# Kernel optimization log

Measured on AMD Instinct MI355X. Metric: run time of the kernel, lower is better.

The kernel has to match this reference:

```python
import jax, jax.numpy as jnp
import numpy as np

N = 8192        # nodes
E = 49152       # edges (~avg degree 6, triangular mesh)
H = 6           # GATv2 heads
C = 512         # hidden_size (per-head out channels)
F_IN = 2 + C    # GATv2 in_channels = coord(2) + hidden(512)
ALL_FEAT = 37   # deform_in_c-2 + 16 + 16
NUM_LOOP = 3
LRELU_SLOPE = 0.2


def setup_inputs() -> dict:
    key = jax.random.key(0)
    ks = jax.random.split(key, 10)
    x = jax.random.uniform(ks[0], (N, 7), dtype=jnp.float32)
    local_feat = jax.random.normal(ks[1], (N, 16), dtype=jnp.float32)
    conv_feat = jax.random.normal(ks[2], (N, 16), dtype=jnp.float32)
    edge_index = jax.random.randint(ks[3], (2, E), 0, N, dtype=jnp.int64)
    bd_mask = jnp.zeros((N,), jnp.int32)  # poly_mesh=False path
    W_lin = jax.random.normal(ks[4], (ALL_FEAT, C), dtype=jnp.float32) / np.float32(np.sqrt(ALL_FEAT))
    b_lin = jnp.zeros((C,), jnp.float32)
    Wl = jax.random.normal(ks[5], (F_IN, H * C), dtype=jnp.float32) / np.float32(np.sqrt(F_IN))
    Wr = jax.random.normal(ks[6], (F_IN, H * C), dtype=jnp.float32) / np.float32(np.sqrt(F_IN))
    att = jax.random.normal(ks[7], (H, C), dtype=jnp.float32) / np.float32(np.sqrt(C))
    gat_bias = jnp.zeros((C,), jnp.float32)
    W_coord = jax.random.normal(ks[8], (C, 2), dtype=jnp.float32) / np.float32(np.sqrt(C))
    b_coord = jnp.zeros((2,), jnp.float32)
    return dict(x=x, local_feat=local_feat, conv_feat=conv_feat,
                W_lin=W_lin, b_lin=b_lin, Wl=Wl, Wr=Wr, att=att,
                gat_bias=gat_bias, W_coord=W_coord, b_coord=b_coord,
                edge_index=edge_index, bd_mask=bd_mask)


def _gatv2(feat, src, dst, Wl, Wr, att, bias):
    # PyG GATv2Conv: lin_l on source, lin_r on target, additive attention
    n = feat.shape[0]
    xl = (feat @ Wl).reshape(n, H, C)            # source-side transform
    xr = (feat @ Wr).reshape(n, H, C)            # target-side transform
    e = xl[src] + xr[dst]                        # [E', H, C]
    e = jax.nn.leaky_relu(e, LRELU_SLOPE)
    logits = jnp.einsum('ehc,hc->eh', e, att)    # [E', H]
    m = jax.ops.segment_max(logits, dst, num_segments=n)
    m = jnp.where(jnp.isfinite(m), m, 0.0)
    a = jnp.exp(logits - m[dst])
    denom = jax.ops.segment_sum(a, dst, num_segments=n) + 1e-16
    alpha = a / denom[dst]                       # segment softmax over incoming edges
    msg = xl[src] * alpha[:, :, None]            # [E', H, C]
    out = jax.ops.segment_sum(msg, dst, num_segments=n)  # [N, H, C]
    return out.mean(axis=1) + bias               # concat=False -> mean over heads


def reference(x, local_feat, conv_feat, W_lin, b_lin, Wl, Wr, att, gat_bias,
              W_coord, b_coord, edge_index, bd_mask):
    coord = x[:, :2]
    hidden_in = jnp.concatenate([x[:, 2:], local_feat, conv_feat], axis=1)
    hidden = jax.nn.selu(hidden_in @ W_lin + b_lin)
    # GATv2Conv adds self-loops by default
    loops = jnp.arange(N, dtype=edge_index.dtype)
    src = jnp.concatenate([edge_index[0], loops])
    dst = jnp.concatenate([edge_index[1], loops])
    for _ in range(NUM_LOOP):
        up = coord[:, 0] == 1.0
        down = coord[:, 0] == 0.0
        left = coord[:, 1] == 0.0
        right = coord[:, 1] == 1.0
        feat = jnp.concatenate([coord, hidden], axis=1)   # [N, 514]
        hidden = jax.nn.selu(_gatv2(feat, src, dst, Wl, Wr, att, gat_bias))
        out = hidden @ W_coord + b_coord                  # [N, 2]
        ox = jnp.where(down, 0.0, jnp.where(up, 1.0, out[:, 0]))
        oy = jnp.where(right, 1.0, jnp.where(left, 0.0, out[:, 1]))
        coord = jnp.stack([ox, oy], axis=1)
    return coord
```

## Files before the change

kernel.cpp:

```cpp
#include <hip/hip_runtime.h>
#include <hip/hip_bf16.h>
#include <math.h>

#define N_NODES   8192
#define NUM_E     49152
#define NUM_EDGES (NUM_E + N_NODES)
#define H_HEADS   6
#define C_DIM     512
#define HC        (H_HEADS * C_DIM)
#define XLR       (2 * HC)
#define N_FEAT    37
#define LRELU_SLOPE 0.2f
#define SELU_LAMBDA 1.0507009873554805f
#define SELU_ALPHA  1.6732632423543772f

typedef __bf16 bf16_t;
typedef bf16_t bf16x8 __attribute__((ext_vector_type(8)));
typedef float  f32x4  __attribute__((ext_vector_type(4)));
typedef float  f32x2  __attribute__((ext_vector_type(2)));

__device__ __forceinline__ int edge_src(const int* ei, int e) {
    return e < NUM_E ? ei[e] : (e - NUM_E);
}
__device__ __forceinline__ int edge_dst(const int* ei, int e) {
    return e < NUM_E ? ei[NUM_E + e] : (e - NUM_E);
}
__device__ __forceinline__ float selu_f(float v) {
    return v > 0.f ? SELU_LAMBDA * v : SELU_LAMBDA * SELU_ALPHA * (__expf(v) - 1.f);
}
__device__ __forceinline__ void gload_lds16(const void* g, void* l) {
    __builtin_amdgcn_global_load_lds((const __attribute__((address_space(1))) void*)g,
                                     (__attribute__((address_space(3))) void*)l, 16, 0, 0);
}

__device__ __forceinline__ float bfly_add64(float s) {
    int t;
    t = __builtin_amdgcn_update_dpp(0, __float_as_int(s), 0xB1,  0xF, 0xF, true);
    s += __int_as_float(t);
    t = __builtin_amdgcn_update_dpp(0, __float_as_int(s), 0x4E,  0xF, 0xF, true);
    s += __int_as_float(t);
    t = __builtin_amdgcn_update_dpp(0, __float_as_int(s), 0x141, 0xF, 0xF, true);
    s += __int_as_float(t);
    t = __builtin_amdgcn_update_dpp(0, __float_as_int(s), 0x140, 0xF, 0xF, true);
    s += __int_as_float(t);
    s += __int_as_float(__builtin_amdgcn_ds_swizzle(__float_as_int(s), 0x401F));
    s += __shfl_xor(s, 32);
    return s;
}

__global__ __launch_bounds__(512) void k_hidden0(
    const float* __restrict__ x, const float* __restrict__ lf,
    const float* __restrict__ cf, const float* __restrict__ W,
    const float* __restrict__ b, bf16_t* __restrict__ hidden,
    float* __restrict__ coord)
{
    int n0 = blockIdx.x * 4;
    int c = threadIdx.x;
    __shared__ float f[4][N_FEAT];
    if (c < 4 * N_FEAT) {
        int m = c / N_FEAT, k = c - m * N_FEAT;
        int n = n0 + m;
        f[m][k] = (k < 5) ? x[n*7 + 2 + k]
                 : (k < 21 ? lf[n*16 + (k - 5)] : cf[n*16 + (k - 21)]);
    }
    if (c < 8) coord[n0*2 + c] = x[(n0 + (c >> 1))*7 + (c & 1)];
    __syncthreads();
    float a0 = b[c], a1 = a0, a2 = a0, a3 = a0;
    #pragma unroll
    for (int k = 0; k < N_FEAT; ++k) {
        float wv = W[k*C_DIM + c];
        a0 = fmaf(f[0][k], wv, a0);
        a1 = fmaf(f[1][k], wv, a1);
        a2 = fmaf(f[2][k], wv, a2);
        a3 = fmaf(f[3][k], wv, a3);
    }
    hidden[(size_t)(n0 + 0)*C_DIM + c] = (bf16_t)selu_f(a0);
    hidden[(size_t)(n0 + 1)*C_DIM + c] = (bf16_t)selu_f(a1);
    hidden[(size_t)(n0 + 2)*C_DIM + c] = (bf16_t)selu_f(a2);
    hidden[(size_t)(n0 + 3)*C_DIM + c] = (bf16_t)selu_f(a3);
}

__global__ __launch_bounds__(256) void k_wt_transpose(const float* __restrict__ W,
                                                      bf16_t* __restrict__ WT)
{
    __shared__ float tile[32][33];
    int k0 = blockIdx.y * 32;
    int n0 = blockIdx.x * 32;
    int tx = threadIdx.x & 31, ty = threadIdx.x >> 5;
    #pragma unroll
    for (int i = 0; i < 4; ++i)
        tile[ty + i*8][tx] = W[(size_t)(k0 + 2 + ty + i*8) * HC + n0 + tx];
    __syncthreads();
    #pragma unroll
    for (int i = 0; i < 4; ++i)
        WT[(size_t)(n0 + ty + i*8) * C_DIM + k0 + tx] = (bf16_t)tile[tx][ty + i*8];
}

__global__ void k_hist(const int* __restrict__ ei, int* __restrict__ counts) {
    int e = blockIdx.x * blockDim.x + threadIdx.x;
    if (e >= NUM_EDGES) return;
    atomicAdd(&counts[edge_dst(ei, e)], 1);
}

__global__ __launch_bounds__(256) void k_scan(const int* __restrict__ counts,
                                              int* __restrict__ row_ptr,
                                              int* __restrict__ cursor) {
    __shared__ int part[256];
    __shared__ int off[257];
    int t = threadIdx.x;
    int base = t * 32;
    int local[32];
    int s = 0;
    #pragma unroll
    for (int i = 0; i < 32; ++i) { local[i] = s; s += counts[base + i]; }
    part[t] = s;
    __syncthreads();
    if (t == 0) {
        off[0] = 0;
        for (int i = 0; i < 256; ++i) off[i+1] = off[i] + part[i];
    }
    __syncthreads();
    int o = off[t];
    #pragma unroll
    for (int i = 0; i < 32; ++i) {
        int v = o + local[i];
        row_ptr[base + i] = v;
        cursor[base + i]  = v;
    }
    if (t == 255) row_ptr[N_NODES] = off[256];
}

__global__ void k_scatter(const int* __restrict__ ei, int* __restrict__ cursor,
                          int* __restrict__ csr_src) {
    int e = blockIdx.x * blockDim.x + threadIdx.x;
    if (e >= NUM_EDGES) return;
    int pos = atomicAdd(&cursor[edge_dst(ei, e)], 1);
    csr_src[pos] = edge_src(ei, e);
}

#define BM 256
#define BN 256
#define BK 64
#define NT (C_DIM / BK)
#define NBX (XLR / BN)
#define NWG ((N_NODES / BM) * NBX)

__global__ __launch_bounds__(512, 2) void k_gemm_bf16(
    const bf16_t* __restrict__ A,
    const bf16_t* __restrict__ BT,
    const float*  __restrict__ Wl,
    const float*  __restrict__ Wr,
    const float*  __restrict__ coord,
    bf16_t* __restrict__ out)
{
    __shared__ __align__(1024) char smem[131072];
    char* sA = smem;
    char* sB = smem + 65536;

    const int tid  = threadIdx.x;
    const int wave = tid >> 6;
    const int lane = tid & 63;
    const int wm   = wave >> 2;
    const int wn   = wave & 3;

    int bid = blockIdx.y * gridDim.x + blockIdx.x;
    bid = (bid & 7) * (NWG / 8) + (bid >> 3);
    const int rowBase = (bid / NBX) * BM;
    const int colBase = (bid % NBX) * BN;

    const int rtid = tid >> 3;
    const int csw  = ((tid & 7) * 8) ^ (((tid >> 3) & 7) << 3);
    const bf16_t* pA = A  + (size_t)(rowBase + rtid) * C_DIM + csw;
    const bf16_t* pB = BT + (size_t)(colBase + rtid) * C_DIM + csw;

    auto stageA = [&](int t, int h) {
        char* l = sA + ((t & 1) << 15) + (h << 14) + (wave << 10);
        const bf16_t* g = pA + (size_t)(h * 128) * C_DIM + t * BK;
        gload_lds16(g,              l);
        gload_lds16(g + 64 * C_DIM, l + 8192);
    };
    auto stageB = [&](int t, int h) {
        char* l = sB + ((t & 1) << 15) + (h << 14) + (wave << 10);
        const bf16_t* g = pB + (size_t)(h * 128) * C_DIM + t * BK;
        gload_lds16(g,              l);
        gload_lds16(g + 64 * C_DIM, l + 8192);
    };

    stageB(0, 0); stageB(0, 1); stageA(0, 0); stageA(0, 1);
    stageB(1, 0); stageB(1, 1);
    __builtin_amdgcn_sched_barrier(0);
    asm volatile("s_waitcnt vmcnt(4)" ::: "memory");
    __builtin_amdgcn_sched_barrier(0);
    asm volatile("s_barrier" ::: "memory");
    __builtin_amdgcn_sched_barrier(0);

    const int kb  = (lane >> 4) << 4;
    const int sw  = (lane & 7) << 4;
    const int xt0 = kb ^ sw;
    const int xt1 = (64 | kb) ^ sw;
    const int aRowOff = (wm * 128 + (lane & 15)) * 128;
    const int bRowOff = (wn * 64  + (lane & 15)) * 128;

    f32x4 acc[8][4] = {};

    #pragma unroll 2
    for (int t = 0; t < NT; ++t) {
        const char* aP = sA + ((t & 1) << 15) + aRowOff;
        const char* bP = sB + ((t & 1) << 15) + bRowOff;
        bf16x8 bfv[4][2];
        bf16x8 af[4][2];

        if (t + 1 < NT) { stageA(t + 1, 0); stageA(t + 1, 1); }
        #pragma unroll
        for (int mf = 0; mf < 4; ++mf) {
            af[mf][0] = *(const bf16x8*)(aP + mf*2048 + xt0);
            af[mf][1] = *(const bf16x8*)(aP + mf*2048 + xt1);
        }
        #pragma unroll
        for (int nf = 0; nf < 4; ++nf) {
            bfv[nf][0] = *(const bf16x8*)(bP + nf * 2048 + xt0);
            bfv[nf][1] = *(const bf16x8*)(bP + nf * 2048 + xt1);
        }
        __builtin_amdgcn_s_setprio(1);
        #pragma unroll
        for (int nf = 0; nf < 4; ++nf)
            #pragma unroll
            for (int mf = 0; mf < 4; ++mf)
                acc[mf][nf] = __builtin_amdgcn_mfma_f32_16x16x32_bf16(af[mf][0], bfv[nf][0], acc[mf][nf], 0, 0, 0);
        #pragma unroll
        for (int nf = 0; nf < 4; ++nf)
            #pragma unroll
            for (int mf = 0; mf < 4; ++mf)
                acc[mf][nf] = __builtin_amdgcn_mfma_f32_16x16x32_bf16(af[mf][1], bfv[nf][1], acc[mf][nf], 0, 0, 0);
        __builtin_amdgcn_s_setprio(0);
        __builtin_amdgcn_sched_barrier(0);
        asm volatile("s_barrier" ::: "memory");
        __builtin_amdgcn_sched_barrier(0);

        if (t + 2 < NT) { stageB(t + 2, 0); stageB(t + 2, 1); }
        #pragma unroll
        for (int mf = 0; mf < 4; ++mf) {
            af[mf][0] = *(const bf16x8*)(aP + (4 + mf)*2048 + xt0);
            af[mf][1] = *(const bf16x8*)(aP + (4 + mf)*2048 + xt1);
        }
        __builtin_amdgcn_s_setprio(1);
        #pragma unroll
        for (int nf = 0; nf < 4; ++nf)
            #pragma unroll
            for (int mf = 0; mf < 4; ++mf)
                acc[4 + mf][nf] = __builtin_amdgcn_mfma_f32_16x16x32_bf16(af[mf][0], bfv[nf][0], acc[4 + mf][nf], 0, 0, 0);
        #pragma unroll
        for (int nf = 0; nf < 4; ++nf)
            #pragma unroll
            for (int mf = 0; mf < 4; ++mf)
                acc[4 + mf][nf] = __builtin_amdgcn_mfma_f32_16x16x32_bf16(af[mf][1], bfv[nf][1], acc[4 + mf][nf], 0, 0, 0);
        __builtin_amdgcn_s_setprio(0);
        __builtin_amdgcn_sched_barrier(0);
        if (t < NT - 2)       asm volatile("s_waitcnt vmcnt(4)" ::: "memory");
        else if (t == NT - 2) asm volatile("s_waitcnt vmcnt(0)" ::: "memory");
        __builtin_amdgcn_sched_barrier(0);
        asm volatile("s_barrier" ::: "memory");
        __builtin_amdgcn_sched_barrier(0);
    }

    const float* Wtop = (colBase < HC) ? Wl : Wr;
    const int coff = (colBase < HC) ? 0 : HC;
    const int ccol  = lane & 15;
    const int crow4 = (lane >> 4) * 4;

    float wv0[4], wv1[4];
    #pragma unroll
    for (int nf = 0; nf < 4; ++nf) {
        int wcol = colBase + wn*64 + nf*16 + ccol - coff;
        wv0[nf] = Wtop[wcol];
        wv1[nf] = Wtop[HC + wcol];
    }
    #pragma unroll
    for (int mf = 0; mf < 8; ++mf) {
        #pragma unroll
        for (int r = 0; r < 4; ++r) {
            int row = rowBase + wm*128 + mf*16 + crow4 + r;
            float c0 = coord[row*2 + 0], c1 = coord[row*2 + 1];
            size_t rb = (size_t)row * XLR;
            #pragma unroll
            for (int nf = 0; nf < 4; ++nf) {
                int col = colBase + wn*64 + nf*16 + ccol;
                out[rb + col] = (bf16_t)(acc[mf][nf][r] + c0 * wv0[nf] + c1 * wv1[nf]);
            }
        }
    }
}

#define MAX_DEG 128
__global__ __launch_bounds__(384, 8) void k_attn_agg(
    const bf16_t* __restrict__ xlr,
    const int* __restrict__ row_ptr, const int* __restrict__ csr_src,
    const float* __restrict__ att,
    const float* __restrict__ gat_bias, const float* __restrict__ W_coord,
    const float* __restrict__ b_coord, const float* __restrict__ coord_in,
    bf16_t* __restrict__ hidden, float* __restrict__ coord_out)
{
    int n = blockIdx.x;
    int tid = threadIdx.x;
    int h = tid >> 6, lane = tid & 63;
    __shared__ int   s_src[MAX_DEG];
    __shared__ float s_acc[HC];
    __shared__ float s_red[12];

    int beg = row_ptr[n];
    int deg = min(row_ptr[n + 1] - beg, MAX_DEG);
    for (int j = tid; j < deg; j += 384) s_src[j] = csr_src[beg + j];
    __syncthreads();

    size_t off = (size_t)h * C_DIM + lane * 8;
    bf16x8 xrv = *(const bf16x8*)(xlr + (size_t)n * XLR + HC + off);
    f32x2 xr2[4], at2[4], ac2[4] = {};
    #pragma unroll
    for (int i = 0; i < 4; ++i) {
        xr2[i] = f32x2{(float)xrv[2*i], (float)xrv[2*i+1]};
        at2[i] = f32x2{att[off + 2*i], att[off + 2*i + 1]};
    }

    float l = 0.f;
    int j = 0;
    for (; j + 2 <= deg; j += 2) {
        bf16x8 xa = *(const bf16x8*)(xlr + (size_t)s_src[j]     * XLR + off);
        bf16x8 xb = *(const bf16x8*)(xlr + (size_t)s_src[j + 1] * XLR + off);
        f32x2 xla[4], xlb[4];
        #pragma unroll
        for (int i = 0; i < 4; ++i) {
            xla[i] = f32x2{(float)xa[2*i], (float)xa[2*i+1]};
            xlb[i] = f32x2{(float)xb[2*i], (float)xb[2*i+1]};
        }
        f32x2 sa = {0.f, 0.f}, sb = {0.f, 0.f};
        #pragma unroll
        for (int i = 0; i < 4; ++i) {
            f32x2 va = xla[i] + xr2[i];
            f32x2 vb = xlb[i] + xr2[i];
            sa += __builtin_elementwise_max(va, va * LRELU_SLOPE) * at2[i];
            sb += __builtin_elementwise_max(vb, vb * LRELU_SLOPE) * at2[i];
        }
        float suma = bfly_add64(sa.x + sa.y);
        float sumb = bfly_add64(sb.x + sb.y);
        float aa = __expf(suma), ab = __expf(sumb);
        l += aa + ab;
        #pragma unroll
        for (int i = 0; i < 4; ++i) ac2[i] += aa * xla[i] + ab * xlb[i];
    }
    if (j < deg) {
        bf16x8 xa = *(const bf16x8*)(xlr + (size_t)s_src[j] * XLR + off);
        f32x2 xla[4];
        #pragma unroll
        for (int i = 0; i < 4; ++i) xla[i] = f32x2{(float)xa[2*i], (float)xa[2*i+1]};
        f32x2 sa = {0.f, 0.f};
        #pragma unroll
        for (int i = 0; i < 4; ++i) {
            f32x2 va = xla[i] + xr2[i];
            sa += __builtin_elementwise_max(va, va * LRELU_SLOPE) * at2[i];
        }
        float suma = bfly_add64(sa.x + sa.y);
        float aa = __expf(suma);
        l += aa;
        #pragma unroll
        for (int i = 0; i < 4; ++i) ac2[i] += aa * xla[i];
    }

    float invl = 1.f / (l + 1e-16f) * (1.f / 6.f);
    #pragma unroll
    for (int i = 0; i < 4; ++i) {
        s_acc[off + 2*i]     = ac2[i].x * invl;
        s_acc[off + 2*i + 1] = ac2[i].y * invl;
    }
    __syncthreads();

    float p0 = 0.f, p1 = 0.f;
    for (int c = tid; c < C_DIM; c += 384) {
        float s = 0.f;
        #pragma unroll
        for (int hh = 0; hh < H_HEADS; ++hh) s += s_acc[hh * C_DIM + c];
        float hv = selu_f(s + gat_bias[c]);
        hidden[n * C_DIM + c] = (bf16_t)hv;
        p0 = fmaf(hv, W_coord[c * 2 + 0], p0);
        p1 = fmaf(hv, W_coord[c * 2 + 1], p1);
    }
    #pragma unroll
    for (int o = 32; o > 0; o >>= 1) { p0 += __shfl_down(p0, o); p1 += __shfl_down(p1, o); }
    if (lane == 0) { s_red[h * 2] = p0; s_red[h * 2 + 1] = p1; }
    __syncthreads();
    if (tid == 0) {
        float o0 = b_coord[0], o1 = b_coord[1];
        #pragma unroll
        for (int w = 0; w < H_HEADS; ++w) { o0 += s_red[w * 2]; o1 += s_red[w * 2 + 1]; }
        float cx = coord_in[n * 2 + 0], cy = coord_in[n * 2 + 1];
        float ox = (cx == 0.0f) ? 0.f : ((cx == 1.0f) ? 1.f : o0);
        float oy = (cy == 1.0f) ? 1.f : ((cy == 0.0f) ? 0.f : o1);
        coord_out[n * 2 + 0] = ox;
        coord_out[n * 2 + 1] = oy;
    }
}

extern "C" void kernel_launch(void* const* d_in, const int* in_sizes, int n_in,
                              void* d_out, int out_size, void* d_ws, size_t ws_size,
                              hipStream_t stream)
{
    const float* x       = (const float*)d_in[0];
    const float* lf      = (const float*)d_in[1];
    const float* cf      = (const float*)d_in[2];
    const float* W_lin   = (const float*)d_in[3];
    const float* b_lin   = (const float*)d_in[4];
    const float* Wl      = (const float*)d_in[5];
    const float* Wr      = (const float*)d_in[6];
    const float* att     = (const float*)d_in[7];
    const float* gbias   = (const float*)d_in[8];
    const float* W_coord = (const float*)d_in[9];
    const float* b_coord = (const float*)d_in[10];
    const int*   ei      = (const int*)d_in[11];

    char* w = (char*)d_ws;
    auto alloc = [&](size_t bytes) { char* p = w; w += (bytes + 255) & ~255ull; return p; };
    bf16_t*   hidden  = (bf16_t*)alloc((size_t)N_NODES * C_DIM * 2);
    bf16_t*   WT      = (bf16_t*)alloc((size_t)XLR * C_DIM * 2);
    bf16_t*   xlr     = (bf16_t*)alloc((size_t)N_NODES * XLR * 2);
    int*      counts  = (int*)alloc((size_t)N_NODES * 4);
    int*      row_ptr = (int*)alloc((size_t)(N_NODES + 1) * 4);
    int*      cursor  = (int*)alloc((size_t)N_NODES * 4);
    int*      csr_src = (int*)alloc((size_t)NUM_EDGES * 4);
    float*    cA      = (float*)alloc((size_t)N_NODES * 2 * 4);
    float*    cB      = (float*)alloc((size_t)N_NODES * 2 * 4);

    hipMemsetAsync(counts, 0, (size_t)N_NODES * 4, stream);
    k_hidden0<<<N_NODES / 4, 512, 0, stream>>>(x, lf, cf, W_lin, b_lin, hidden, cA);
    {
        dim3 tg(HC / 32, C_DIM / 32);
        k_wt_transpose<<<tg, 256, 0, stream>>>(Wl, WT);
        k_wt_transpose<<<tg, 256, 0, stream>>>(Wr, WT + (size_t)HC * C_DIM);
    }
    k_hist<<<(NUM_EDGES + 255) / 256, 256, 0, stream>>>(ei, counts);
    k_scan<<<1, 256, 0, stream>>>(counts, row_ptr, cursor);
    k_scatter<<<(NUM_EDGES + 255) / 256, 256, 0, stream>>>(ei, cursor, csr_src);

    float* cin = cA;
    for (int it = 0; it < 3; ++it) {
        float* cout = (it == 2) ? (float*)d_out : ((it == 0) ? cB : cA);
        dim3 g(NBX, N_NODES / BM);
        k_gemm_bf16<<<g, 512, 0, stream>>>(hidden, WT, Wl, Wr, cin, xlr);
        k_attn_agg<<<N_NODES, 384, 0, stream>>>(xlr, row_ptr, csr_src, att,
                                                gbias, W_coord, b_coord, cin, hidden, cout);
        cin = cout;
    }
}
```

Baseline: 484.1 us.

## Make GEMM persistent and prefetch next tile during epilogue

The GEMM launch becomes a fixed grid of 256 persistent workgroups, each looping over three output tiles with the same swizzled tile mapping as before. After the K loop of one tile finishes, the first two K-stages of the next tile are issued as global-to-LDS loads before the current tile's epilogue (bias from coord and the bf16 stores). The aim is to hide the epilogue and the next tile's prologue latency behind each other and to avoid launching and ramping up three waves of workgroups. The epilogue's own global loads and stores now share the vmcnt counter with the prefetches, so the next tile's first wait may stall longer than strictly needed.

```diff
diff --git a/kernel.cpp b/kernel.cpp
--- a/kernel.cpp
+++ b/kernel.cpp
@@ -144,6 +144,8 @@
 #define NT (C_DIM / BK)
 #define NBX (XLR / BN)
 #define NWG ((N_NODES / BM) * NBX)
+#define GEMM_BLOCKS 256
+#define ASSIGN (NWG / GEMM_BLOCKS)
 
 __global__ __launch_bounds__(512, 2) void k_gemm_bf16(
     const bf16_t* __restrict__ A,
@@ -163,15 +165,19 @@
     const int wm   = wave >> 2;
     const int wn   = wave & 3;
 
-    int bid = blockIdx.y * gridDim.x + blockIdx.x;
-    bid = (bid & 7) * (NWG / 8) + (bid >> 3);
-    const int rowBase = (bid / NBX) * BM;
-    const int colBase = (bid % NBX) * BN;
-
     const int rtid = tid >> 3;
     const int csw  = ((tid & 7) * 8) ^ (((tid >> 3) & 7) << 3);
-    const bf16_t* pA = A  + (size_t)(rowBase + rtid) * C_DIM + csw;
-    const bf16_t* pB = BT + (size_t)(colBase + rtid) * C_DIM + csw;
+
+    int rowBase, colBase;
+    const bf16_t *pA, *pB;
+    auto mapTile = [&](int a) {
+        int tile = blockIdx.x + a * GEMM_BLOCKS;
+        int swz  = (tile & 7) * (NWG / 8) + (tile >> 3);
+        rowBase = (swz / NBX) * BM;
+        colBase = (swz % NBX) * BN;
+        pA = A  + (size_t)(rowBase + rtid) * C_DIM + csw;
+        pB = BT + (size_t)(colBase + rtid) * C_DIM + csw;
+    };
 
     auto stageA = [&](int t, int h) {
         char* l = sA + ((t & 1) << 15) + (h << 14) + (wave << 10);
@@ -186,106 +192,118 @@
         gload_lds16(g + 64 * C_DIM, l + 8192);
     };
 
-    stageB(0, 0); stageB(0, 1); stageA(0, 0); stageA(0, 1);
-    stageB(1, 0); stageB(1, 1);
-    __builtin_amdgcn_sched_barrier(0);
-    asm volatile("s_waitcnt vmcnt(4)" ::: "memory");
-    __builtin_amdgcn_sched_barrier(0);
-    asm volatile("s_barrier" ::: "memory");
-    __builtin_amdgcn_sched_barrier(0);
-
     const int kb  = (lane >> 4) << 4;
     const int sw  = (lane & 7) << 4;
     const int xt0 = kb ^ sw;
     const int xt1 = (64 | kb) ^ sw;
     const int aRowOff = (wm * 128 + (lane & 15)) * 128;
     const int bRowOff = (wn * 64  + (lane & 15)) * 128;
-
-    f32x4 acc[8][4] = {};
-
-    #pragma unroll 2
-    for (int t = 0; t < NT; ++t) {
-        const char* aP = sA + ((t & 1) << 15) + aRowOff;
-        const char* bP = sB + ((t & 1) << 15) + bRowOff;
-        bf16x8 bfv[4][2];
-        bf16x8 af[4][2];
-
-        if (t + 1 < NT) { stageA(t + 1, 0); stageA(t + 1, 1); }
-        #pragma unroll
-        for (int mf = 0; mf < 4; ++mf) {
-            af[mf][0] = *(const bf16x8*)(aP + mf*2048 + xt0);
-            af[mf][1] = *(const bf16x8*)(aP + mf*2048 + xt1);
-        }
-        #pragma unroll
-        for (int nf = 0; nf < 4; ++nf) {
-            bfv[nf][0] = *(const bf16x8*)(bP + nf * 2048 + xt0);
-            bfv[nf][1] = *(const bf16x8*)(bP + nf * 2048 + xt1);
-        }
-        __builtin_amdgcn_s_setprio(1);
-        #pragma unroll
-        for (int nf = 0; nf < 4; ++nf)
-            #pragma unroll
-            for (int mf = 0; mf < 4; ++mf)
-                acc[mf][nf] = __builtin_amdgcn_mfma_f32_16x16x32_bf16(af[mf][0], bfv[nf][0], acc[mf][nf], 0, 0, 0);
-        #pragma unroll
-        for (int nf = 0; nf < 4; ++nf)
-            #pragma unroll
-            for (int mf = 0; mf < 4; ++mf)
-                acc[mf][nf] = __builtin_amdgcn_mfma_f32_16x16x32_bf16(af[mf][1], bfv[nf][1], acc[mf][nf], 0, 0, 0);
-        __builtin_amdgcn_s_setprio(0);
+    const int ccol  = lane & 15;
+    const int crow4 = (lane >> 4) * 4;
+
+    mapTile(0);
+    stageB(0, 0); stageB(0, 1); stageA(0, 0); stageA(0, 1);
+    stageB(1, 0); stageB(1, 1);
+
+    for (int a = 0; a < ASSIGN; ++a) {
+        const int rowBaseE = rowBase, colBaseE = colBase;
+
+        __builtin_amdgcn_sched_barrier(0);
+        asm volatile("s_waitcnt vmcnt(4)" ::: "memory");
         __builtin_amdgcn_sched_barrier(0);
         asm volatile("s_barrier" ::: "memory");
         __builtin_amdgcn_sched_barrier(0);
 
-        if (t + 2 < NT) { stageB(t + 2, 0); stageB(t + 2, 1); }
-        #pragma unroll
-        for (int mf = 0; mf < 4; ++mf) {
-            af[mf][0] = *(const bf16x8*)(aP + (4 + mf)*2048 + xt0);
-            af[mf][1] = *(const bf16x8*)(aP + (4 + mf)*2048 + xt1);
-        }
-        __builtin_amdgcn_s_setprio(1);
-        #pragma unroll
-        for (int nf = 0; nf < 4; ++nf)
-            #pragma unroll
-            for (int mf = 0; mf < 4; ++mf)
-                acc[4 + mf][nf] = __builtin_amdgcn_mfma_f32_16x16x32_bf16(af[mf][0], bfv[nf][0], acc[4 + mf][nf], 0, 0, 0);
-        #pragma unroll
-        for (int nf = 0; nf < 4; ++nf)
-            #pragma unroll
-            for (int mf = 0; mf < 4; ++mf)
-                acc[4 + mf][nf] = __builtin_amdgcn_mfma_f32_16x16x32_bf16(af[mf][1], bfv[nf][1], acc[4 + mf][nf], 0, 0, 0);
-        __builtin_amdgcn_s_setprio(0);
-        __builtin_amdgcn_sched_barrier(0);
-        if (t < NT - 2)       asm volatile("s_waitcnt vmcnt(4)" ::: "memory");
-        else if (t == NT - 2) asm volatile("s_waitcnt vmcnt(0)" ::: "memory");
-        __builtin_amdgcn_sched_barrier(0);
-        asm volatile("s_barrier" ::: "memory");
-        __builtin_amdgcn_sched_barrier(0);
-    }
-
-    const float* Wtop = (colBase < HC) ? Wl : Wr;
-    const int coff = (colBase < HC) ? 0 : HC;
-    const int ccol  = lane & 15;
-    const int crow4 = (lane >> 4) * 4;
-
-    float wv0[4], wv1[4];
-    #pragma unroll
-    for (int nf = 0; nf < 4; ++nf) {
-        int wcol = colBase + wn*64 + nf*16 + ccol - coff;
-        wv0[nf] = Wtop[wcol];
-        wv1[nf] = Wtop[HC + wcol];
-    }
-    #pragma unroll
-    for (int mf = 0; mf < 8; ++mf) {
-        #pragma unroll
-        for (int r = 0; r < 4; ++r) {
-            int row = rowBase + wm*128 + mf*16 + crow4 + r;
-            float c0 = coord[row*2 + 0], c1 = coord[row*2 + 1];
-            size_t rb = (size_t)row * XLR;
+        f32x4 acc[8][4] = {};
+
+        #pragma unroll 2
+        for (int t = 0; t < NT; ++t) {
+            const char* aP = sA + ((t & 1) << 15) + aRowOff;
+            const char* bP = sB + ((t & 1) << 15) + bRowOff;
+            bf16x8 bfv[4][2];
+            bf16x8 af[4][2];
+
+            if (t + 1 < NT) { stageA(t + 1, 0); stageA(t + 1, 1); }
+            #pragma unroll
+            for (int mf = 0; mf < 4; ++mf) {
+                af[mf][0] = *(const bf16x8*)(aP + mf*2048 + xt0);
+                af[mf][1] = *(const bf16x8*)(aP + mf*2048 + xt1);
+            }
             #pragma unroll
             for (int nf = 0; nf < 4; ++nf) {
-                int col = colBase + wn*64 + nf*16 + ccol;
-                out[rb + col] = (bf16_t)(acc[mf][nf][r] + c0 * wv0[nf] + c1 * wv1[nf]);
+                bfv[nf][0] = *(const bf16x8*)(bP + nf * 2048 + xt0);
+                bfv[nf][1] = *(const bf16x8*)(bP + nf * 2048 + xt1);
+            }
+            __builtin_amdgcn_s_setprio(1);
+            #pragma unroll
+            for (int nf = 0; nf < 4; ++nf)
+                #pragma unroll
+                for (int mf = 0; mf < 4; ++mf)
+                    acc[mf][nf] = __builtin_amdgcn_mfma_f32_16x16x32_bf16(af[mf][0], bfv[nf][0], acc[mf][nf], 0, 0, 0);
+            #pragma unroll
+            for (int nf = 0; nf < 4; ++nf)
+                #pragma unroll
+                for (int mf = 0; mf < 4; ++mf)
+                    acc[mf][nf] = __builtin_amdgcn_mfma_f32_16x16x32_bf16(af[mf][1], bfv[nf][1], acc[mf][nf], 0, 0, 0);
+            __builtin_amdgcn_s_setprio(0);
+            __builtin_amdgcn_sched_barrier(0);
+            asm volatile("s_barrier" ::: "memory");
+            __builtin_amdgcn_sched_barrier(0);
+
+            if (t + 2 < NT) { stageB(t + 2, 0); stageB(t + 2, 1); }
+            #pragma unroll
+            for (int mf = 0; mf < 4; ++mf) {
+                af[mf][0] = *(const bf16x8*)(aP + (4 + mf)*2048 + xt0);
+                af[mf][1] = *(const bf16x8*)(aP + (4 + mf)*2048 + xt1);
+            }
+            __builtin_amdgcn_s_setprio(1);
+            #pragma unroll
+            for (int nf = 0; nf < 4; ++nf)
+                #pragma unroll
+                for (int mf = 0; mf < 4; ++mf)
+                    acc[4 + mf][nf] = __builtin_amdgcn_mfma_f32_16x16x32_bf16(af[mf][0], bfv[nf][0], acc[4 + mf][nf], 0, 0, 0);
+            #pragma unroll
+            for (int nf = 0; nf < 4; ++nf)
+                #pragma unroll
+                for (int mf = 0; mf < 4; ++mf)
+                    acc[4 + mf][nf] = __builtin_amdgcn_mfma_f32_16x16x32_bf16(af[mf][1], bfv[nf][1], acc[4 + mf][nf], 0, 0, 0);
+            __builtin_amdgcn_s_setprio(0);
+            __builtin_amdgcn_sched_barrier(0);
+            if (t < NT - 2)       asm volatile("s_waitcnt vmcnt(4)" ::: "memory");
+            else if (t == NT - 2) asm volatile("s_waitcnt vmcnt(0)" ::: "memory");
+            __builtin_amdgcn_sched_barrier(0);
+            asm volatile("s_barrier" ::: "memory");
+            __builtin_amdgcn_sched_barrier(0);
+        }
+
+        if (a + 1 < ASSIGN) {
+            mapTile(a + 1);
+            stageB(0, 0); stageB(0, 1); stageA(0, 0); stageA(0, 1);
+            stageB(1, 0); stageB(1, 1);
+        }
+
+        const float* Wtop = (colBaseE < HC) ? Wl : Wr;
+        const int coff = (colBaseE < HC) ? 0 : HC;
+
+        float wv0[4], wv1[4];
+        #pragma unroll
+        for (int nf = 0; nf < 4; ++nf) {
+            int wcol = colBaseE + wn*64 + nf*16 + ccol - coff;
+            wv0[nf] = Wtop[wcol];
+            wv1[nf] = Wtop[HC + wcol];
+        }
+        #pragma unroll
+        for (int mf = 0; mf < 8; ++mf) {
+            #pragma unroll
+            for (int r = 0; r < 4; ++r) {
+                int row = rowBaseE + wm*128 + mf*16 + crow4 + r;
+                float c0 = coord[row*2 + 0], c1 = coord[row*2 + 1];
+                size_t rb = (size_t)row * XLR;
+                #pragma unroll
+                for (int nf = 0; nf < 4; ++nf) {
+                    int col = colBaseE + wn*64 + nf*16 + ccol;
+                    out[rb + col] = (bf16_t)(acc[mf][nf][r] + c0 * wv0[nf] + c1 * wv1[nf]);
+                }
             }
         }
     }
@@ -442,8 +460,7 @@
     float* cin = cA;
     for (int it = 0; it < 3; ++it) {
         float* cout = (it == 2) ? (float*)d_out : ((it == 0) ? cB : cA);
-        dim3 g(NBX, N_NODES / BM);
-        k_gemm_bf16<<<g, 512, 0, stream>>>(hidden, WT, Wl, Wr, cin, xlr);
+        k_gemm_bf16<<<GEMM_BLOCKS, 512, 0, stream>>>(hidden, WT, Wl, Wr, cin, xlr);
         k_attn_agg<<<N_NODES, 384, 0, stream>>>(xlr, row_ptr, csr_src, att,
                                                 gbias, W_coord, b_coord, cin, hidden, cout);
         cin = cout;
```

Measured after the change: 494.2 us. 1.02x slower.

## Shrink GEMM tile to 128x128 with simpler double-buffer and XCD-aware block mapping

Applied to the files above, without the earlier changes.

The xl/xr projection GEMM tile shrinks from 256x256 to 128x128, which halves LDS use and raises the occupancy hint to 4 workgroups per CU. The prefetch pipeline becomes a simple double buffer that loads A and B together and waits for all loads each step. Block-to-tile mapping is rewritten so each XCD handles a contiguous band of row tiles. This gives more workgroups and better load balance in exchange for less operand reuse per tile and a shallower prefetch that exposes more memory latency.

```diff
diff --git a/kernel.cpp b/kernel.cpp
--- a/kernel.cpp
+++ b/kernel.cpp
@@ -138,14 +138,14 @@
     csr_src[pos] = edge_src(ei, e);
 }
 
-#define BM 256
-#define BN 256
+#define BM 128
+#define BN 128
 #define BK 64
 #define NT (C_DIM / BK)
 #define NBX (XLR / BN)
 #define NWG ((N_NODES / BM) * NBX)
 
-__global__ __launch_bounds__(512, 2) void k_gemm_bf16(
+__global__ __launch_bounds__(512, 4) void k_gemm_bf16(
     const bf16_t* __restrict__ A,
     const bf16_t* __restrict__ BT,
     const float*  __restrict__ Wl,
@@ -153,9 +153,9 @@
     const float*  __restrict__ coord,
     bf16_t* __restrict__ out)
 {
-    __shared__ __align__(1024) char smem[131072];
+    __shared__ __align__(1024) char smem[65536];
     char* sA = smem;
-    char* sB = smem + 65536;
+    char* sB = smem + 32768;
 
     const int tid  = threadIdx.x;
     const int wave = tid >> 6;
@@ -163,33 +163,33 @@
     const int wm   = wave >> 2;
     const int wn   = wave & 3;
 
-    int bid = blockIdx.y * gridDim.x + blockIdx.x;
-    bid = (bid & 7) * (NWG / 8) + (bid >> 3);
-    const int rowBase = (bid / NBX) * BM;
-    const int colBase = (bid % NBX) * BN;
+    int bid = blockIdx.x;
+    int xcd = bid & 7;
+    int loc = bid >> 3;
+    const int rowBase = (xcd * 8 + (loc & 7)) * BM;
+    const int colBase = (loc >> 3) * BN;
 
     const int rtid = tid >> 3;
     const int csw  = ((tid & 7) * 8) ^ (((tid >> 3) & 7) << 3);
     const bf16_t* pA = A  + (size_t)(rowBase + rtid) * C_DIM + csw;
     const bf16_t* pB = BT + (size_t)(colBase + rtid) * C_DIM + csw;
 
-    auto stageA = [&](int t, int h) {
-        char* l = sA + ((t & 1) << 15) + (h << 14) + (wave << 10);
-        const bf16_t* g = pA + (size_t)(h * 128) * C_DIM + t * BK;
+    auto stageA = [&](int t) {
+        char* l = sA + ((t & 1) << 14) + (wave << 10);
+        const bf16_t* g = pA + t * BK;
         gload_lds16(g,              l);
         gload_lds16(g + 64 * C_DIM, l + 8192);
     };
-    auto stageB = [&](int t, int h) {
-        char* l = sB + ((t & 1) << 15) + (h << 14) + (wave << 10);
-        const bf16_t* g = pB + (size_t)(h * 128) * C_DIM + t * BK;
+    auto stageB = [&](int t) {
+        char* l = sB + ((t & 1) << 14) + (wave << 10);
+        const bf16_t* g = pB + t * BK;
         gload_lds16(g,              l);
         gload_lds16(g + 64 * C_DIM, l + 8192);
     };
 
-    stageB(0, 0); stageB(0, 1); stageA(0, 0); stageA(0, 1);
-    stageB(1, 0); stageB(1, 1);
+    stageA(0); stageB(0);
     __builtin_amdgcn_sched_barrier(0);
-    asm volatile("s_waitcnt vmcnt(4)" ::: "memory");
+    asm volatile("s_waitcnt vmcnt(0)" ::: "memory");
     __builtin_amdgcn_sched_barrier(0);
     asm volatile("s_barrier" ::: "memory");
     __builtin_amdgcn_sched_barrier(0);
@@ -198,66 +198,44 @@
     const int sw  = (lane & 7) << 4;
     const int xt0 = kb ^ sw;
     const int xt1 = (64 | kb) ^ sw;
-    const int aRowOff = (wm * 128 + (lane & 15)) * 128;
-    const int bRowOff = (wn * 64  + (lane & 15)) * 128;
-
-    f32x4 acc[8][4] = {};
+    const int aRowOff = (wm * 64 + (lane & 15)) * 128;
+    const int bRowOff = (wn * 32 + (lane & 15)) * 128;
+
+    f32x4 acc[4][2] = {};
 
     #pragma unroll 2
     for (int t = 0; t < NT; ++t) {
-        const char* aP = sA + ((t & 1) << 15) + aRowOff;
-        const char* bP = sB + ((t & 1) << 15) + bRowOff;
-        bf16x8 bfv[4][2];
-        bf16x8 af[4][2];
-
-        if (t + 1 < NT) { stageA(t + 1, 0); stageA(t + 1, 1); }
+        const char* aP = sA + ((t & 1) << 14) + aRowOff;
+        const char* bP = sB + ((t & 1) << 14) + bRowOff;
+
+        if (t + 1 < NT) { stageA(t + 1); stageB(t + 1); }
+
+        bf16x8 af[4][2], bfv[2][2];
         #pragma unroll
         for (int mf = 0; mf < 4; ++mf) {
             af[mf][0] = *(const bf16x8*)(aP + mf*2048 + xt0);
             af[mf][1] = *(const bf16x8*)(aP + mf*2048 + xt1);
         }
         #pragma unroll
-        for (int nf = 0; nf < 4; ++nf) {
-            bfv[nf][0] = *(const bf16x8*)(bP + nf * 2048 + xt0);
-            bfv[nf][1] = *(const bf16x8*)(bP + nf * 2048 + xt1);
+        for (int nf = 0; nf < 2; ++nf) {
+            bfv[nf][0] = *(const bf16x8*)(bP + nf*2048 + xt0);
+            bfv[nf][1] = *(const bf16x8*)(bP + nf*2048 + xt1);
         }
         __builtin_amdgcn_s_setprio(1);
         #pragma unroll
-        for (int nf = 0; nf < 4; ++nf)
+        for (int nf = 0; nf < 2; ++nf)
             #pragma unroll
             for (int mf = 0; mf < 4; ++mf)
                 acc[mf][nf] = __builtin_amdgcn_mfma_f32_16x16x32_bf16(af[mf][0], bfv[nf][0], acc[mf][nf], 0, 0, 0);
         #pragma unroll
-        for (int nf = 0; nf < 4; ++nf)
+        for (int nf = 0; nf < 2; ++nf)
             #pragma unroll
             for (int mf = 0; mf < 4; ++mf)
                 acc[mf][nf] = __builtin_amdgcn_mfma_f32_16x16x32_bf16(af[mf][1], bfv[nf][1], acc[mf][nf], 0, 0, 0);
         __builtin_amdgcn_s_setprio(0);
+
         __builtin_amdgcn_sched_barrier(0);
-        asm volatile("s_barrier" ::: "memory");
-        __builtin_amdgcn_sched_barrier(0);
-
-        if (t + 2 < NT) { stageB(t + 2, 0); stageB(t + 2, 1); }
-        #pragma unroll
-        for (int mf = 0; mf < 4; ++mf) {
-            af[mf][0] = *(const bf16x8*)(aP + (4 + mf)*2048 + xt0);
-            af[mf][1] = *(const bf16x8*)(aP + (4 + mf)*2048 + xt1);
-        }
-        __builtin_amdgcn_s_setprio(1);
-        #pragma unroll
-        for (int nf = 0; nf < 4; ++nf)
-            #pragma unroll
-            for (int mf = 0; mf < 4; ++mf)
-                acc[4 + mf][nf] = __builtin_amdgcn_mfma_f32_16x16x32_bf16(af[mf][0], bfv[nf][0], acc[4 + mf][nf], 0, 0, 0);
-        #pragma unroll
-        for (int nf = 0; nf < 4; ++nf)
-            #pragma unroll
-            for (int mf = 0; mf < 4; ++mf)
-                acc[4 + mf][nf] = __builtin_amdgcn_mfma_f32_16x16x32_bf16(af[mf][1], bfv[nf][1], acc[4 + mf][nf], 0, 0, 0);
-        __builtin_amdgcn_s_setprio(0);
-        __builtin_amdgcn_sched_barrier(0);
-        if (t < NT - 2)       asm volatile("s_waitcnt vmcnt(4)" ::: "memory");
-        else if (t == NT - 2) asm volatile("s_waitcnt vmcnt(0)" ::: "memory");
+        asm volatile("s_waitcnt vmcnt(0)" ::: "memory");
         __builtin_amdgcn_sched_barrier(0);
         asm volatile("s_barrier" ::: "memory");
         __builtin_amdgcn_sched_barrier(0);
@@ -268,23 +246,23 @@
     const int ccol  = lane & 15;
     const int crow4 = (lane >> 4) * 4;
 
-    float wv0[4], wv1[4];
-    #pragma unroll
-    for (int nf = 0; nf < 4; ++nf) {
-        int wcol = colBase + wn*64 + nf*16 + ccol - coff;
+    float wv0[2], wv1[2];
+    #pragma unroll
+    for (int nf = 0; nf < 2; ++nf) {
+        int wcol = colBase + wn*32 + nf*16 + ccol - coff;
         wv0[nf] = Wtop[wcol];
         wv1[nf] = Wtop[HC + wcol];
     }
     #pragma unroll
-    for (int mf = 0; mf < 8; ++mf) {
+    for (int mf = 0; mf < 4; ++mf) {
         #pragma unroll
         for (int r = 0; r < 4; ++r) {
-            int row = rowBase + wm*128 + mf*16 + crow4 + r;
+            int row = rowBase + wm*64 + mf*16 + crow4 + r;
             float c0 = coord[row*2 + 0], c1 = coord[row*2 + 1];
             size_t rb = (size_t)row * XLR;
             #pragma unroll
-            for (int nf = 0; nf < 4; ++nf) {
-                int col = colBase + wn*64 + nf*16 + ccol;
+            for (int nf = 0; nf < 2; ++nf) {
+                int col = colBase + wn*32 + nf*16 + ccol;
                 out[rb + col] = (bf16_t)(acc[mf][nf][r] + c0 * wv0[nf] + c1 * wv1[nf]);
             }
         }
@@ -442,8 +420,7 @@
     float* cin = cA;
     for (int it = 0; it < 3; ++it) {
         float* cout = (it == 2) ? (float*)d_out : ((it == 0) ? cB : cA);
-        dim3 g(NBX, N_NODES / BM);
-        k_gemm_bf16<<<g, 512, 0, stream>>>(hidden, WT, Wl, Wr, cin, xlr);
+        k_gemm_bf16<<<NWG, 512, 0, stream>>>(hidden, WT, Wl, Wr, cin, xlr);
         k_attn_agg<<<N_NODES, 384, 0, stream>>>(xlr, row_ptr, csr_src, att,
                                                 gbias, W_coord, b_coord, cin, hidden, cout);
         cin = cout;
```

After: 511.4 us. 1.06x slower.
